# Kernel optimization log

Measured on AMD Instinct MI355X. Metric: run time of the kernel, lower is better.

The kernel has to match this reference:

```python
import jax, jax.numpy as jnp
import numpy as np

TOPK = 4  # constructor default topk=4


def setup_inputs() -> dict:
    key = jax.random.key(0)
    k_x, k_a, k_b, k_w, k_bias = jax.random.split(key, 5)
    b, s, h, j, a, r = 4, 2048, 2048, 2048, 64, 16
    x = jax.random.normal(k_x, (b, s, h), dtype=jnp.float32)
    A = jax.random.normal(k_a, (a, r, h), dtype=jnp.float32) * 0.02   # adapter down-proj bank
    B = jax.random.normal(k_b, (a, j, r), dtype=jnp.float32) * 0.02   # adapter up-proj bank
    W = jax.random.normal(k_w, (j, h), dtype=jnp.float32) * 0.02      # base Linear weight
    bias = jax.random.normal(k_bias, (j,), dtype=jnp.float32) * 0.02  # base Linear bias
    return {"x": x, "A": A, "B": B, "W": W, "bias": bias}


def reference(x, A, B, W, bias):
    # vecs: per-adapter low-rank projections of each token. [b,s,a,r]
    vecs = jnp.einsum('arh,bsh->bsar', A, x)
    # routing score = L2 norm over rank dim. [b,s,a]
    arrows = jnp.linalg.norm(vecs, axis=-1)
    # top-k adapters per token -> uniform 1/topk routing weights (scatter of a constant,
    # so no gradient flows through the routing weights, matching torch semantics).
    _, idx = jax.lax.top_k(arrows, TOPK)                     # [b,s,topk]
    routes = jax.nn.one_hot(idx, arrows.shape[-1], dtype=x.dtype).sum(-2) / TOPK  # [b,s,a]
    # weighted combine of selected adapter vecs. [b,s,r]
    v = jnp.einsum('bsa,bsar->bsr', routes, vecs)
    # delta = (routes-weighted B) applied to v; contract over a then r without
    # materializing the [b,s,j,r] intermediate. [b,s,j]
    delta = jnp.einsum('bsa,ajr,bsr->bsj', routes, B, v)
    base = jnp.einsum('bsh,jh->bsj', x, W) + bias
    return base + delta
```

## Files before the change

kernel.cpp:

```cpp
#include <hip/hip_runtime.h>
#include <hip/hip_bf16.h>
#include <stdint.h>

#define TOKENS 8192
#define H 2048
#define JDIM 2048
#define NADAPT 64
#define RANK 16
#define KG 1024
#define KTOT 3072

typedef __bf16 v8bf __attribute__((ext_vector_type(8)));
typedef float v4f __attribute__((ext_vector_type(4)));
typedef unsigned short us8 __attribute__((ext_vector_type(8)));
typedef unsigned short us4 __attribute__((ext_vector_type(4)));

__device__ __forceinline__ unsigned short f2bf(float f) {
  union { __bf16 b; unsigned short u; } c; c.b = (__bf16)f; return c.u;
}
__device__ __forceinline__ float bf2f(unsigned short u) {
  union { unsigned int u; float f; } c; c.u = ((unsigned int)u) << 16; return c.f;
}

__device__ __forceinline__ us8 pack8(float4 a, float4 b) {
  us8 r;
  r[0]=f2bf(a.x); r[1]=f2bf(a.y); r[2]=f2bf(a.z); r[3]=f2bf(a.w);
  r[4]=f2bf(b.x); r[5]=f2bf(b.y); r[6]=f2bf(b.z); r[7]=f2bf(b.w);
  return r;
}

__device__ __forceinline__ void split8(float4 a, float4 b, us8& h, us8& l) {
  float v[8] = {a.x, a.y, a.z, a.w, b.x, b.y, b.z, b.w};
  #pragma unroll
  for (int i = 0; i < 8; ++i) {
    h[i] = f2bf(v[i]);
    l[i] = f2bf(v[i] - bf2f(h[i]));
  }
}

__global__ void cast_x_split_kernel(const float* __restrict__ x,
                                    unsigned short* __restrict__ XG,
                                    unsigned short* __restrict__ XLO) {
  int idx = blockIdx.x * 256 + threadIdx.x;
  int row = idx >> 8;
  int cg  = idx & 255;
  const float4* s = (const float4*)(x + ((size_t)row << 11) + ((size_t)cg << 3));
  float4 a = s[0], b = s[1];
  us8 h, l;
  split8(a, b, h, l);
  *(us8*)(XG  + (size_t)row * KTOT + ((size_t)cg << 3)) = h;
  *(us8*)(XLO + (size_t)row * H    + ((size_t)cg << 3)) = l;
}

__global__ void cast_a_split_kernel(const float* __restrict__ A,
                                    unsigned short* __restrict__ Ahi,
                                    unsigned short* __restrict__ Alo) {
  int idx = blockIdx.x * 256 + threadIdx.x;
  int row = idx >> 8;
  int cg  = idx & 255;
  const float4* s = (const float4*)(A + ((size_t)row << 11) + ((size_t)cg << 3));
  float4 a = s[0], b = s[1];
  us8 h, l;
  split8(a, b, h, l);
  *(us8*)(Ahi + (size_t)row * H + ((size_t)cg << 3)) = h;
  *(us8*)(Alo + (size_t)row * H + ((size_t)cg << 3)) = l;
}

__global__ void cast2048_kernel(const float* __restrict__ src,
                                unsigned short* __restrict__ dst, int dstld) {
  int idx = blockIdx.x * 256 + threadIdx.x;
  int row = idx >> 8;
  int cg  = idx & 255;
  const float4* s = (const float4*)(src + ((size_t)row << 11) + ((size_t)cg << 3));
  float4 a = s[0], b = s[1];
  *(us8*)(dst + (size_t)row * dstld + ((size_t)cg << 3)) = pack8(a, b);
}

__global__ void cast_b_kernel(const float* __restrict__ Bsrc,
                              unsigned short* __restrict__ WB) {
  int idx = blockIdx.x * 256 + threadIdx.x;
  int a = idx >> 11, j = idx & 2047;
  const float4* s = (const float4*)(Bsrc + (((size_t)a << 11) + j) * RANK);
  float4 f0 = s[0], f1 = s[1], f2 = s[2], f3 = s[3];
  us8* d = (us8*)(WB + (size_t)j * KTOT + H + a * RANK);
  d[0] = pack8(f0, f1);
  d[1] = pack8(f2, f3);
}

__global__ void route_kernel(const float* __restrict__ vecs,
                             unsigned short* __restrict__ XG) {
  __shared__ float vsh[4][16];
  int wave = threadIdx.x >> 6, lane = threadIdx.x & 63;
  int t = blockIdx.x * 4 + wave;
  const float* vrow = vecs + (size_t)t * KG;
  const float4* vp = (const float4*)(vrow + lane * RANK);
  float4 q0 = vp[0], q1 = vp[1], q2 = vp[2], q3 = vp[3];
  float ss = q0.x*q0.x + q0.y*q0.y + q0.z*q0.z + q0.w*q0.w
           + q1.x*q1.x + q1.y*q1.y + q1.z*q1.z + q1.w*q1.w
           + q2.x*q2.x + q2.y*q2.y + q2.z*q2.z + q2.w*q2.w
           + q3.x*q3.x + q3.y*q3.y + q3.z*q3.z + q3.w*q3.w;
  float arr = ss;
  int sel[4];
  #pragma unroll
  for (int k = 0; k < 4; ++k) {
    float m = arr; int mi = lane;
    #pragma unroll
    for (int o = 32; o > 0; o >>= 1) {
      float om = __shfl_xor(m, o);
      int oi  = __shfl_xor(mi, o);
      if (om > m || (om == m && oi < mi)) { m = om; mi = oi; }
    }
    sel[k] = mi;
    if (lane == mi) arr = -3.0e38f;
  }
  if (lane < 16) {
    float s = vrow[sel[0]*RANK + lane] + vrow[sel[1]*RANK + lane]
            + vrow[sel[2]*RANK + lane] + vrow[sel[3]*RANK + lane];
    vsh[wave][lane] = 0.0625f * s;
  }
  __syncthreads();
  bool on = (lane == sel[0]) | (lane == sel[1]) | (lane == sel[2]) | (lane == sel[3]);
  us8 lo, hi;
  #pragma unroll
  for (int r = 0; r < 8; ++r) lo[r] = on ? f2bf(vsh[wave][r])     : (unsigned short)0;
  #pragma unroll
  for (int r = 0; r < 8; ++r) hi[r] = on ? f2bf(vsh[wave][r + 8]) : (unsigned short)0;
  us8* d = (us8*)(XG + (size_t)t * KTOT + H + lane * RANK);
  d[0] = lo; d[1] = hi;
}

__device__ __forceinline__ void gload_lds16(const void* gsrc, void* ldst) {
  __builtin_amdgcn_global_load_lds(
      (const __attribute__((address_space(1))) unsigned int*)gsrc,
      (__attribute__((address_space(3))) unsigned int*)ldst, 16, 0, 0);
}

__global__ __launch_bounds__(256, 2) void gemm1_kernel(
    const unsigned short* __restrict__ Xhi,
    const unsigned short* __restrict__ Xlo,
    const unsigned short* __restrict__ Ahi,
    const unsigned short* __restrict__ Alo,
    float* __restrict__ C) {
  __shared__ unsigned short AsH[128 * 32];
  __shared__ unsigned short AsL[128 * 32];
  __shared__ unsigned short BsH[128 * 32];
  __shared__ unsigned short BsL[128 * 32];
  const int tid = threadIdx.x;
  const int lane = tid & 63, wave = tid >> 6;
  const int wr = wave >> 1, wc = wave & 1;
  const int bm = blockIdx.x, bn = blockIdx.y;

  v4f acc[4][4];
  #pragma unroll
  for (int i = 0; i < 4; ++i)
    #pragma unroll
    for (int j = 0; j < 4; ++j)
      acc[i][j] = (v4f){0.f, 0.f, 0.f, 0.f};

  const unsigned short* XhiB = Xhi + (size_t)(bm * 128) * KTOT;
  const unsigned short* XloB = Xlo + (size_t)(bm * 128) * H;
  const unsigned short* AhiB = Ahi + (size_t)(bn * 128) * H;
  const unsigned short* AloB = Alo + (size_t)(bn * 128) * H;

  const int rA = lane & 15;
  const int kk = (lane >> 4) << 3;

  for (int k0 = 0; k0 < H; k0 += 32) {
    #pragma unroll
    for (int rnd = 0; rnd < 2; ++rnd) {
      int e = rnd * 256 + tid;
      int r = e >> 2, c8 = (e & 3) << 3;
      gload_lds16(XhiB + (size_t)r * KTOT + k0 + c8, (char*)AsH + (size_t)e * 16);
      gload_lds16(XloB + (size_t)r * H    + k0 + c8, (char*)AsL + (size_t)e * 16);
      gload_lds16(AhiB + (size_t)r * H    + k0 + c8, (char*)BsH + (size_t)e * 16);
      gload_lds16(AloB + (size_t)r * H    + k0 + c8, (char*)BsL + (size_t)e * 16);
    }
    __syncthreads();
    v8bf ah[4], al[4], bh[4], bl[4];
    #pragma unroll
    for (int i = 0; i < 4; ++i) {
      ah[i] = *(const v8bf*)&AsH[(wr * 64 + i * 16 + rA) * 32 + kk];
      al[i] = *(const v8bf*)&AsL[(wr * 64 + i * 16 + rA) * 32 + kk];
    }
    #pragma unroll
    for (int j = 0; j < 4; ++j) {
      bh[j] = *(const v8bf*)&BsH[(wc * 64 + j * 16 + rA) * 32 + kk];
      bl[j] = *(const v8bf*)&BsL[(wc * 64 + j * 16 + rA) * 32 + kk];
    }
    #pragma unroll
    for (int i = 0; i < 4; ++i)
      #pragma unroll
      for (int j = 0; j < 4; ++j) {
        acc[i][j] = __builtin_amdgcn_mfma_f32_16x16x32_bf16(ah[i], bh[j], acc[i][j], 0, 0, 0);
        acc[i][j] = __builtin_amdgcn_mfma_f32_16x16x32_bf16(ah[i], bl[j], acc[i][j], 0, 0, 0);
        acc[i][j] = __builtin_amdgcn_mfma_f32_16x16x32_bf16(al[i], bh[j], acc[i][j], 0, 0, 0);
      }
    __syncthreads();
  }

  const int rowbase = bm * 128 + wr * 64;
  const int colbase = bn * 128 + wc * 64;
  #pragma unroll
  for (int i = 0; i < 4; ++i) {
    int r0 = rowbase + i * 16 + ((lane >> 4) << 2);
    #pragma unroll
    for (int j = 0; j < 4; ++j) {
      int col = colbase + j * 16 + (lane & 15);
      #pragma unroll
      for (int q = 0; q < 4; ++q)
        C[(size_t)(r0 + q) * KG + col] = acc[i][j][q];
    }
  }
}

__global__ __launch_bounds__(256, 2) void gemm_bt_kernel(
    const unsigned short* __restrict__ A, const unsigned short* __restrict__ Bt,
    float* __restrict__ C, const float* __restrict__ bias,
    int K, int lda, int ldb, int ldc) {
  __shared__ unsigned short As[128 * 32];
  __shared__ unsigned short Bs[128 * 32];
  const int tid = threadIdx.x;
  const int lane = tid & 63, wave = tid >> 6;
  const int wr = wave >> 1, wc = wave & 1;
  const int bm = blockIdx.x, bn = blockIdx.y;

  v4f acc[4][4];
  #pragma unroll
  for (int i = 0; i < 4; ++i)
    #pragma unroll
    for (int j = 0; j < 4; ++j)
      acc[i][j] = (v4f){0.f, 0.f, 0.f, 0.f};

  const unsigned short* Abase = A + (size_t)(bm * 128) * lda;
  const unsigned short* Bbase = Bt + (size_t)(bn * 128) * ldb;

  const int rA = lane & 15;
  const int kk = (lane >> 4) << 3;

  for (int k0 = 0; k0 < K; k0 += 32) {
    #pragma unroll
    for (int rnd = 0; rnd < 2; ++rnd) {
      int e = rnd * 256 + tid;
      int r = e >> 2, c8 = (e & 3) << 3;
      gload_lds16(Abase + (size_t)r * lda + k0 + c8, (char*)As + (size_t)e * 16);
      gload_lds16(Bbase + (size_t)r * ldb + k0 + c8, (char*)Bs + (size_t)e * 16);
    }
    __syncthreads();
    v8bf af[4], bfr[4];
    #pragma unroll
    for (int i = 0; i < 4; ++i)
      af[i] = *(const v8bf*)&As[(wr * 64 + i * 16 + rA) * 32 + kk];
    #pragma unroll
    for (int j = 0; j < 4; ++j)
      bfr[j] = *(const v8bf*)&Bs[(wc * 64 + j * 16 + rA) * 32 + kk];
    #pragma unroll
    for (int i = 0; i < 4; ++i)
      #pragma unroll
      for (int j = 0; j < 4; ++j)
        acc[i][j] = __builtin_amdgcn_mfma_f32_16x16x32_bf16(af[i], bfr[j], acc[i][j], 0, 0, 0);
    __syncthreads();
  }

  const int rowbase = bm * 128 + wr * 64;
  const int colbase = bn * 128 + wc * 64;
  #pragma unroll
  for (int i = 0; i < 4; ++i) {
    int r0 = rowbase + i * 16 + ((lane >> 4) << 2);
    #pragma unroll
    for (int j = 0; j < 4; ++j) {
      int col = colbase + j * 16 + (lane & 15);
      float bv = bias ? bias[col] : 0.f;
      #pragma unroll
      for (int q = 0; q < 4; ++q)
        C[(size_t)(r0 + q) * ldc + col] = acc[i][j][q] + bv;
    }
  }
}

extern "C" void kernel_launch(void* const* d_in, const int* in_sizes, int n_in,
                              void* d_out, int out_size, void* d_ws, size_t ws_size,
                              hipStream_t stream) {
  const float* x    = (const float*)d_in[0];
  const float* A    = (const float*)d_in[1];
  const float* Bb   = (const float*)d_in[2];
  const float* W    = (const float*)d_in[3];
  const float* bias = (const float*)d_in[4];
  float* out = (float*)d_out;

  char* ws = (char*)d_ws;
  unsigned short* XG  = (unsigned short*)ws;
  unsigned short* WB  = (unsigned short*)(ws + (size_t)48 * 1024 * 1024);
  unsigned short* Ahi = (unsigned short*)(ws + (size_t)60 * 1024 * 1024);
  unsigned short* Alo = (unsigned short*)(ws + (size_t)64 * 1024 * 1024);
  float* vecs         = (float*)d_out;
  unsigned short* XLO = (unsigned short*)((char*)d_out + (size_t)32 * 1024 * 1024);

  cast_x_split_kernel<<<TOKENS, 256, 0, stream>>>(x, XG, XLO);
  cast_a_split_kernel<<<KG / 1, 256, 0, stream>>>(A, Ahi, Alo);
  cast2048_kernel<<<JDIM, 256, 0, stream>>>(W, WB, KTOT);
  cast_b_kernel<<<512, 256, 0, stream>>>(Bb, WB);

  gemm1_kernel<<<dim3(TOKENS / 128, KG / 128), 256, 0, stream>>>(
      XG, XLO, Ahi, Alo, vecs);

  route_kernel<<<TOKENS / 4, 256, 0, stream>>>(vecs, XG);

  gemm_bt_kernel<<<dim3(TOKENS / 128, JDIM / 128), 256, 0, stream>>>(
      XG, WB, out, bias, KTOT, KTOT, KTOT, 2048);
}
```

Before: 264.7 us.

## Replace final GEMM with 256x256-tile, 8-phase pipelined LDS kernel

Replaces the 128x128 single-buffered output GEMM with a 512-thread kernel that computes 256x256 tiles. It uses a 4-slot LDS ring with async global-to-LDS loads interleaved across eight MFMA phases, an XOR swizzle to avoid bank conflicts, and setprio around the MFMA bursts. The goal is to hide global load latency behind matrix math and raise data reuse per tile. In exchange it uses 128KB of LDS and one block per CU. The grid drops to 256 blocks, which may underfill the CUs and leaves correctness dependent on hand-tuned waitcnt counts.

```diff
diff --git a/kernel.cpp b/kernel.cpp
--- a/kernel.cpp
+++ b/kernel.cpp
@@ -9,6 +9,7 @@
 #define RANK 16
 #define KG 1024
 #define KTOT 3072
+#define NT2 48
 
 typedef __bf16 v8bf __attribute__((ext_vector_type(8)));
 typedef float v4f __attribute__((ext_vector_type(4)));
@@ -213,68 +214,115 @@
   }
 }
 
-__global__ __launch_bounds__(256, 2) void gemm_bt_kernel(
-    const unsigned short* __restrict__ A, const unsigned short* __restrict__ Bt,
-    float* __restrict__ C, const float* __restrict__ bias,
-    int K, int lda, int ldb, int ldc) {
-  __shared__ unsigned short As[128 * 32];
-  __shared__ unsigned short Bs[128 * 32];
+#define BAR() asm volatile("s_waitcnt lgkmcnt(0)\n\ts_barrier" ::: "memory")
+#define VM8() asm volatile("s_waitcnt vmcnt(8)" ::: "memory")
+
+#define STAGE(regionUS, panel, kelem) do {                                        \
+  gload_lds16((panel) + aoff0 + (kelem), (char*)(regionUS) + tid * 16);           \
+  gload_lds16((panel) + aoff1 + (kelem), (char*)(regionUS) + 8192 + tid * 16);    \
+} while (0)
+
+#define PHASE(mh, RAr, RBr, ISSUE, DOVM) do {                                     \
+  if ((mh) == 0) {                                                                \
+    _Pragma("unroll")                                                             \
+    for (int j = 0; j < 4; ++j)                                                   \
+      bfr[j] = *(const v8bf*)((const char*)(RBr) + bbyte + j * 1024);             \
+  }                                                                               \
+  _Pragma("unroll")                                                               \
+  for (int i = 0; i < 4; ++i)                                                     \
+    af[i] = *(const v8bf*)((const char*)(RAr) + abyte + ((mh)*4 + i) * 1024);     \
+  ISSUE;                                                                          \
+  BAR();                                                                          \
+  __builtin_amdgcn_s_setprio(1);                                                  \
+  _Pragma("unroll")                                                               \
+  for (int i = 0; i < 4; ++i)                                                     \
+    _Pragma("unroll")                                                             \
+    for (int j = 0; j < 4; ++j)                                                   \
+      acc[(mh)*4 + i][j] = __builtin_amdgcn_mfma_f32_16x16x32_bf16(               \
+          af[i], bfr[j], acc[(mh)*4 + i][j], 0, 0, 0);                            \
+  __builtin_amdgcn_s_setprio(0);                                                  \
+  DOVM;                                                                           \
+  BAR();                                                                          \
+} while (0)
+
+__global__ __launch_bounds__(512, 1) void gemm2_8ph_kernel(
+    const unsigned short* __restrict__ Xg, const unsigned short* __restrict__ Wb,
+    float* __restrict__ C, const float* __restrict__ bias) {
+  __shared__ unsigned short lds[65536];
   const int tid = threadIdx.x;
-  const int lane = tid & 63, wave = tid >> 6;
-  const int wr = wave >> 1, wc = wave & 1;
-  const int bm = blockIdx.x, bn = blockIdx.y;
-
-  v4f acc[4][4];
-  #pragma unroll
-  for (int i = 0; i < 4; ++i)
+  const int lane = tid & 63, wid = tid >> 6;
+  const int wr = wid >> 2, wc = wid & 3;
+  const int rA = lane & 15, grp = lane >> 4;
+  const int grpx = (grp ^ (rA & 3)) << 4;
+
+  const int bid = blockIdx.x;
+  const int bn = bid & 7, bm = bid >> 3;
+
+  const unsigned short* Ap = Xg + (size_t)(bm * 256) * KTOT;
+  const unsigned short* Bp = Wb + (size_t)(bn * 256) * KTOT;
+
+  const int srow = tid >> 2;
+  const int scol = ((tid & 3) ^ ((tid >> 2) & 3)) << 3;
+  const size_t aoff0 = (size_t)srow * KTOT + scol;
+  const size_t aoff1 = (size_t)(srow + 128) * KTOT + scol;
+
+  unsigned short* A0k0 = lds;
+  unsigned short* A0k1 = lds + 8192;
+  unsigned short* B0k0 = lds + 16384;
+  unsigned short* B0k1 = lds + 24576;
+  unsigned short* A1k0 = lds + 32768;
+  unsigned short* A1k1 = lds + 40960;
+  unsigned short* B1k0 = lds + 49152;
+  unsigned short* B1k1 = lds + 57344;
+
+  const int abyte = (wr * 128 + rA) * 64 + grpx;
+  const int bbyte = (wc * 64 + rA) * 64 + grpx;
+
+  v4f acc[8][4];
+  #pragma unroll
+  for (int i = 0; i < 8; ++i)
     #pragma unroll
     for (int j = 0; j < 4; ++j)
       acc[i][j] = (v4f){0.f, 0.f, 0.f, 0.f};
-
-  const unsigned short* Abase = A + (size_t)(bm * 128) * lda;
-  const unsigned short* Bbase = Bt + (size_t)(bn * 128) * ldb;
-
-  const int rA = lane & 15;
-  const int kk = (lane >> 4) << 3;
-
-  for (int k0 = 0; k0 < K; k0 += 32) {
-    #pragma unroll
-    for (int rnd = 0; rnd < 2; ++rnd) {
-      int e = rnd * 256 + tid;
-      int r = e >> 2, c8 = (e & 3) << 3;
-      gload_lds16(Abase + (size_t)r * lda + k0 + c8, (char*)As + (size_t)e * 16);
-      gload_lds16(Bbase + (size_t)r * ldb + k0 + c8, (char*)Bs + (size_t)e * 16);
-    }
-    __syncthreads();
-    v8bf af[4], bfr[4];
-    #pragma unroll
-    for (int i = 0; i < 4; ++i)
-      af[i] = *(const v8bf*)&As[(wr * 64 + i * 16 + rA) * 32 + kk];
+  v8bf af[4], bfr[4];
+
+  STAGE(A0k0, Ap, 0);
+  STAGE(B0k0, Bp, 0);
+  STAGE(A0k1, Ap, 32);
+  STAGE(B0k1, Bp, 32);
+  STAGE(A1k0, Ap, 64);
+  STAGE(B1k0, Bp, 64);
+  VM8();
+  BAR();
+
+  #pragma unroll 1
+  for (int t = 0; t < NT2; t += 2) {
+    const int k1a = (t + 1) * 64 + 32;
+    const int k0a = (t + 2 < NT2 ? t + 2 : NT2 - 1) * 64;
+    const int k1b = (t + 2 < NT2 ? t + 2 : NT2 - 1) * 64 + 32;
+    const int k0b = (t + 3 < NT2 ? t + 3 : NT2 - 1) * 64;
+    PHASE(0, A0k0, B0k0, STAGE(A1k1, Ap, k1a), ((void)0));
+    PHASE(1, A0k0, B0k0, STAGE(B1k1, Bp, k1a), VM8());
+    PHASE(0, A0k1, B0k1, STAGE(A0k0, Ap, k0a), ((void)0));
+    PHASE(1, A0k1, B0k1, STAGE(B0k0, Bp, k0a), VM8());
+    PHASE(0, A1k0, B1k0, STAGE(A0k1, Ap, k1b), ((void)0));
+    PHASE(1, A1k0, B1k0, STAGE(B0k1, Bp, k1b), VM8());
+    PHASE(0, A1k1, B1k1, STAGE(A1k0, Ap, k0b), ((void)0));
+    PHASE(1, A1k1, B1k1, STAGE(B1k0, Bp, k0b), VM8());
+  }
+
+  const int row0 = bm * 256 + wr * 128 + (grp << 2);
+  const int col0 = bn * 256 + wc * 64 + rA;
+  float bv[4];
+  #pragma unroll
+  for (int j = 0; j < 4; ++j) bv[j] = bias[col0 + j * 16];
+  #pragma unroll
+  for (int mi = 0; mi < 8; ++mi)
     #pragma unroll
     for (int j = 0; j < 4; ++j)
-      bfr[j] = *(const v8bf*)&Bs[(wc * 64 + j * 16 + rA) * 32 + kk];
-    #pragma unroll
-    for (int i = 0; i < 4; ++i)
-      #pragma unroll
-      for (int j = 0; j < 4; ++j)
-        acc[i][j] = __builtin_amdgcn_mfma_f32_16x16x32_bf16(af[i], bfr[j], acc[i][j], 0, 0, 0);
-    __syncthreads();
-  }
-
-  const int rowbase = bm * 128 + wr * 64;
-  const int colbase = bn * 128 + wc * 64;
-  #pragma unroll
-  for (int i = 0; i < 4; ++i) {
-    int r0 = rowbase + i * 16 + ((lane >> 4) << 2);
-    #pragma unroll
-    for (int j = 0; j < 4; ++j) {
-      int col = colbase + j * 16 + (lane & 15);
-      float bv = bias ? bias[col] : 0.f;
       #pragma unroll
       for (int q = 0; q < 4; ++q)
-        C[(size_t)(r0 + q) * ldc + col] = acc[i][j][q] + bv;
-    }
-  }
+        C[(size_t)(row0 + mi * 16 + q) * JDIM + col0 + j * 16] = acc[mi][j][q] + bv[j];
 }
 
 extern "C" void kernel_launch(void* const* d_in, const int* in_sizes, int n_in,
@@ -305,6 +353,5 @@
 
   route_kernel<<<TOKENS / 4, 256, 0, stream>>>(vecs, XG);
 
-  gemm_bt_kernel<<<dim3(TOKENS / 128, JDIM / 128), 256, 0, stream>>>(
-      XG, WB, out, bias, KTOT, KTOT, KTOT, 2048);
-}
+  gemm2_8ph_kernel<<<256, 512, 0, stream>>>(XG, WB, out, bias);
+}
```

Measured after the change: 246.3 us. 1.07x faster.
